# Kernel optimization log

Measured on AMD Instinct MI355X. Metric: run time of the kernel, lower is better.

## Reference

```python
import jax, jax.numpy as jnp
import numpy as np

EPS = 1e-7
MAX_SQDIST = 50.0
K_NEG = 75  # self.nsn / neg_num
GAMMA = 1.0

N_NODES = 30000
DIM = 128
T_LINKS = 3000


def _minkowski_dot(x, y):
    # x, y: (..., d) -> (...,)
    return -x[..., 0] * y[..., 0] + jnp.sum(x[..., 1:] * y[..., 1:], axis=-1)


def _sqdist(x, y, c):
    # Hyperboloid squared distance (HGCN manifolds.Hyperboloid.sqdist)
    K = 1.0 / c
    theta = jnp.clip(-_minkowski_dot(x, y) / K, 1.0 + EPS)
    return jnp.minimum(K * jnp.arccosh(theta) ** 2, MAX_SQDIST)


def _sqdist_all(qx, emb, c):
    # qx: (t, d) queries vs all emb: (N, d) -> (t, N)
    prod = -jnp.outer(qx[:, 0], emb[:, 0]) + qx[:, 1:] @ emb[:, 1:].T
    K = 1.0 / c
    theta = jnp.clip(-prod / K, 1.0 + EPS)
    return jnp.minimum(K * jnp.arccosh(theta) ** 2, MAX_SQDIST)


def setup_inputs() -> dict:
    key = jax.random.key(0)
    k1, k2 = jax.random.split(key)
    embeddings = jax.random.normal(k1, (N_NODES, DIM), dtype=jnp.float32)
    c = jnp.ones((1,), dtype=jnp.float32)
    train_links = jax.random.randint(k2, (T_LINKS, 2), 0, N_NODES, dtype=jnp.int64)
    return {"embeddings": embeddings, "c": c, "train_links": train_links}


def reference(embeddings, c, train_links):
    cs = c[0]
    t = train_links.shape[0]
    k = K_NEG
    left = train_links[:, 0]
    right = train_links[:, 1]
    left_x = embeddings[left]    # (t, d)
    right_x = embeddings[right]  # (t, d)

    # positive sqdist + margin
    D = _sqdist(left_x, right_x, cs) + GAMMA  # (t,)

    # hardest negatives: k nearest nodes to each query (ascending sqdist)
    def knn_idx(qx):
        sq = _sqdist_all(qx, embeddings, cs)       # (t, N)
        _, idx = jax.lax.top_k(-sq, k)             # smallest-k distances
        return idx                                  # (t, k)

    neg_right = knn_idx(left_x)   # negatives replacing right entity
    neg2_left = knn_idx(right_x)  # negatives replacing left entity

    # B = sqdist(left, neg_right); L1 = relu(D - B)
    B = _sqdist(left_x[:, None, :], embeddings[neg_right], cs)   # (t, k)
    L1 = jax.nn.relu(D[:, None] - B)

    # E = sqdist(neg2_left, right); L2 = relu(D - E)
    E = _sqdist(embeddings[neg2_left], right_x[:, None, :], cs)  # (t, k)
    L2 = jax.nn.relu(D[:, None] - E)

    return (jnp.sum(L1) + jnp.sum(L2)) / (2.0 * k * t)
```

## Files before the change

kernel.cpp:

```cpp
#include <hip/hip_runtime.h>
#include <hip/hip_fp16.h>
#include <hip/hip_bf16.h>

#define TL 3000
#define NN 30000
#define DIM 128
#define KNEG 75
#define NQL (2 * TL)
#define EPSF 1e-7f
#define MAXSQ 50.0f

#define ESUB 512
#define ECH 256
#define NCH (ESUB / ECH)
#define QT 64
#define QBLK 94
#define FLAGTH 125

typedef __attribute__((ext_vector_type(8))) short bf16x8;
typedef __attribute__((ext_vector_type(4))) float f32x4;

__device__ __forceinline__ int wred_i(int v) {
#pragma unroll
  for (int o = 32; o > 0; o >>= 1) v += __shfl_xor(v, o, 64);
  return v;
}
__device__ __forceinline__ float wred_f(float v) {
#pragma unroll
  for (int o = 32; o > 0; o >>= 1) v += __shfl_xor(v, o, 64);
  return v;
}

__device__ __forceinline__ float sqdist_f(float prod, float cv, float K) {
  float theta = fmaxf(-prod * cv, 1.0f + EPSF);
  float a = acoshf(theta);
  return fminf(K * a * a, MAXSQ);
}

__device__ __forceinline__ unsigned short to_bf16(float x) {
  __hip_bfloat16 h = __float2bfloat16(x);
  return *(unsigned short*)&h;
}

__launch_bounds__(256)
__global__ void gemm_cf(const float* __restrict__ emb, const float* __restrict__ c,
                        const int* __restrict__ links, float* __restrict__ partial,
                        int* __restrict__ nf, int* __restrict__ list) {
  __shared__ __align__(16) unsigned short Es[ECH * DIM];
  const int tid = threadIdx.x;
  const int lane = tid & 63;
  const int w = tid >> 6;
  const int am = lane & 15;
  const int aq = lane >> 4;
  const int qt = blockIdx.x;
  const float cv = c[0];
  const float K = 1.0f / cv;
  const float thresh = -(1.0f + EPSF) / cv;

  bf16x8 A[4][4];
#pragma unroll
  for (int mg = 0; mg < 4; ++mg) {
    int q = qt * QT + mg * 16 + am;
    int node = 0;
    if (q < NQL) {
      int li = (q < TL) ? q : q - TL;
      node = (q < TL) ? links[2 * li] : links[2 * li + 1];
    }
    const float* qr = emb + (size_t)node * DIM;
#pragma unroll
    for (int kc = 0; kc < 4; ++kc) {
      float4 f0 = *(const float4*)(qr + kc * 32 + aq * 8);
      float4 f1 = *(const float4*)(qr + kc * 32 + aq * 8 + 4);
      if (kc == 0 && aq == 0) f0.x = -f0.x;
      bf16x8 v;
      v[0] = (short)to_bf16(f0.x); v[1] = (short)to_bf16(f0.y);
      v[2] = (short)to_bf16(f0.z); v[3] = (short)to_bf16(f0.w);
      v[4] = (short)to_bf16(f1.x); v[5] = (short)to_bf16(f1.y);
      v[6] = (short)to_bf16(f1.z); v[7] = (short)to_bf16(f1.w);
      A[mg][kc] = v;
    }
  }

  int cnt[4][4];
#pragma unroll
  for (int mg = 0; mg < 4; ++mg)
#pragma unroll
    for (int r = 0; r < 4; ++r) cnt[mg][r] = 0;

  for (int ch = 0; ch < NCH; ++ch) {
#pragma unroll
    for (int i = 0; i < 16; ++i) {
      int g = w * 16 + i;
      int sg = g >> 2, kc = g & 3;
      const float* src = emb + (size_t)(ch * ECH + sg * 16 + am) * DIM + kc * 32 + aq * 8;
      float4 f0 = *(const float4*)src;
      float4 f1 = *(const float4*)(src + 4);
      bf16x8 v;
      v[0] = (short)to_bf16(f0.x); v[1] = (short)to_bf16(f0.y);
      v[2] = (short)to_bf16(f0.z); v[3] = (short)to_bf16(f0.w);
      v[4] = (short)to_bf16(f1.x); v[5] = (short)to_bf16(f1.y);
      v[6] = (short)to_bf16(f1.z); v[7] = (short)to_bf16(f1.w);
      *(bf16x8*)&Es[(g * 64 + lane) * 8] = v;
    }
    __syncthreads();
#pragma unroll
    for (int s = 0; s < 4; ++s) {
      int sg = w * 4 + s;
      f32x4 a0 = {0.f, 0.f, 0.f, 0.f}, a1 = {0.f, 0.f, 0.f, 0.f};
      f32x4 a2 = {0.f, 0.f, 0.f, 0.f}, a3 = {0.f, 0.f, 0.f, 0.f};
#pragma unroll
      for (int kc = 0; kc < 4; ++kc) {
        bf16x8 B = *(const bf16x8*)&Es[((sg * 4 + kc) * 64 + lane) * 8];
        a0 = __builtin_amdgcn_mfma_f32_16x16x32_bf16(A[0][kc], B, a0, 0, 0, 0);
        a1 = __builtin_amdgcn_mfma_f32_16x16x32_bf16(A[1][kc], B, a1, 0, 0, 0);
        a2 = __builtin_amdgcn_mfma_f32_16x16x32_bf16(A[2][kc], B, a2, 0, 0, 0);
        a3 = __builtin_amdgcn_mfma_f32_16x16x32_bf16(A[3][kc], B, a3, 0, 0, 0);
      }
#pragma unroll
      for (int r = 0; r < 4; ++r) {
        cnt[0][r] += (a0[r] >= thresh);
        cnt[1][r] += (a1[r] >= thresh);
        cnt[2][r] += (a2[r] >= thresh);
        cnt[3][r] += (a3[r] >= thresh);
      }
    }
    __syncthreads();
  }

  int* lc = (int*)&Es[0];
  if (tid < QT + 1) lc[tid] = 0;
  __syncthreads();
#pragma unroll
  for (int mg = 0; mg < 4; ++mg)
#pragma unroll
    for (int r = 0; r < 4; ++r) {
      int v = cnt[mg][r];
      v += __shfl_xor(v, 1, 64);
      v += __shfl_xor(v, 2, 64);
      v += __shfl_xor(v, 4, 64);
      v += __shfl_xor(v, 8, 64);
      if (am == 0) atomicAdd(&lc[mg * 16 + aq * 4 + r], v);
    }
  __syncthreads();

  if (tid < QT) {
    float contrib = 0.f;
    int q = qt * QT + tid;
    if (q < NQL) {
      int li = (q < TL) ? q : q - TL;
      long l = links[2 * li];
      long r = links[2 * li + 1];
      const float4* x = (const float4*)(emb + l * DIM);
      const float4* y = (const float4*)(emb + r * DIM);
      float dot = 0.f, x0 = 0.f, y0 = 0.f;
#pragma unroll
      for (int k = 0; k < 32; ++k) {
        float4 a = x[k], b = y[k];
        if (k == 0) { x0 = a.x; y0 = b.x; }
        dot = fmaf(a.x, b.x, dot);
        dot = fmaf(a.y, b.y, dot);
        dot = fmaf(a.z, b.z, dot);
        dot = fmaf(a.w, b.w, dot);
      }
      float Dq = sqdist_f(dot - 2.0f * x0 * y0, cv, K) + 1.0f;
      float acl = acoshf(1.0f + EPSF);
      float clipv = fminf(K * acl * acl, MAXSQ);
      if (lc[tid] >= FLAGTH) {
        contrib = (float)KNEG * fmaxf(Dq - clipv, 0.f);
      } else {
        int p = atomicAdd(&lc[QT], 1);
        list[qt * QT + p] = q;
      }
    }
    contrib = wred_f(contrib);
    if (tid == 0) partial[qt] = contrib * (1.0f / (2.0f * (float)KNEG * (float)TL));
  }
  __syncthreads();
  if (tid == 0) nf[qt] = lc[QT];
}

__launch_bounds__(256)
__global__ void final_kernel(const float* __restrict__ emb, const float* __restrict__ c,
                             const int* __restrict__ links, const float* __restrict__ partial,
                             const int* __restrict__ nf, const int* __restrict__ list,
                             float* __restrict__ out) {
  __shared__ __align__(16) float qvec[DIM];
  __shared__ unsigned short s16[NN];
  __shared__ int ish[4];
  __shared__ float fsh[4];
  __shared__ float acc_total;
  const int tid = threadIdx.x;

  float t = (tid < QBLK) ? partial[tid] : 0.f;
  t = wred_f(t);
  if ((tid & 63) == 0) fsh[tid >> 6] = t;
  __syncthreads();
  if (tid == 0) acc_total = fsh[0] + fsh[1] + fsh[2] + fsh[3];
  __syncthreads();

  const float cv = c[0];
  const float K = 1.0f / cv;

  for (int qt = 0; qt < QBLK; ++qt) {
    int n = nf[qt];
    for (int j = 0; j < n; ++j) {
      const int q = list[qt * QT + j];
      const int li = (q < TL) ? q : q - TL;
      const int node = (q < TL) ? links[2 * li] : links[2 * li + 1];

      float Dq;
      {
        long l = links[2 * li];
        long r = links[2 * li + 1];
        const float4* x = (const float4*)(emb + l * DIM);
        const float4* y = (const float4*)(emb + r * DIM);
        float dot = 0.f, x0 = 0.f, y0 = 0.f;
#pragma unroll
        for (int k = 0; k < 32; ++k) {
          float4 a = x[k], b = y[k];
          if (k == 0) { x0 = a.x; y0 = b.x; }
          dot = fmaf(a.x, b.x, dot);
          dot = fmaf(a.y, b.y, dot);
          dot = fmaf(a.z, b.z, dot);
          dot = fmaf(a.w, b.w, dot);
        }
        Dq = sqdist_f(dot - 2.0f * x0 * y0, cv, K) + 1.0f;
      }

      if (tid < DIM) qvec[tid] = emb[(long)node * DIM + tid];
      __syncthreads();
      const float q0 = qvec[0];
      const float4* q4 = (const float4*)qvec;

      for (int jj = tid; jj < NN; jj += 256) {
        const float4* row = (const float4*)(emb + (long)jj * DIM);
        float acc = 0.f, e0 = 0.f;
#pragma unroll
        for (int k = 0; k < DIM / 4; ++k) {
          float4 e = row[k];
          float4 v = q4[k];
          if (k == 0) e0 = e.x;
          acc = fmaf(e.x, v.x, acc);
          acc = fmaf(e.y, v.y, acc);
          acc = fmaf(e.z, v.z, acc);
          acc = fmaf(e.w, v.w, acc);
        }
        float s = sqdist_f(acc - 2.0f * e0 * q0, cv, K);
        s16[jj] = __half_as_ushort(__float2half_rn(s));
      }
      __syncthreads();

      unsigned int lo = 0, hi = 0xFFFFu;
      while (lo < hi) {
        unsigned int mid = (lo + hi) >> 1;
        int cnt = 0;
        for (int jj = tid; jj < NN; jj += 256) cnt += (s16[jj] <= mid) ? 1 : 0;
        cnt = wred_i(cnt);
        if ((tid & 63) == 0) ish[tid >> 6] = cnt;
        __syncthreads();
        int tot = ish[0] + ish[1] + ish[2] + ish[3];
        if (tot >= KNEG) hi = mid; else lo = mid + 1;
        __syncthreads();
      }
      const unsigned int T = lo;
      const float Tval = __half2float(__ushort_as_half((unsigned short)T));

      int nl = 0;
      float sum = 0.f;
      for (int jj = tid; jj < NN; jj += 256) {
        unsigned short k = s16[jj];
        if ((unsigned int)k < T) {
          nl++;
          sum += fmaxf(Dq - __half2float(__ushort_as_half(k)), 0.f);
        }
      }
      nl = wred_i(nl);
      sum = wred_f(sum);
      if ((tid & 63) == 0) { ish[tid >> 6] = nl; fsh[tid >> 6] = sum; }
      __syncthreads();
      if (tid == 0) {
        int n_less = ish[0] + ish[1] + ish[2] + ish[3];
        float s = fsh[0] + fsh[1] + fsh[2] + fsh[3];
        s += (float)(KNEG - n_less) * fmaxf(Dq - Tval, 0.f);
        acc_total += s * (1.0f / (2.0f * (float)KNEG * (float)TL));
      }
      __syncthreads();
    }
  }
  if (tid == 0) out[0] = acc_total;
}

extern "C" void kernel_launch(void* const* d_in, const int* in_sizes, int n_in,
                              void* d_out, int out_size, void* d_ws, size_t ws_size,
                              hipStream_t stream) {
  const float* emb = (const float*)d_in[0];
  const float* c = (const float*)d_in[1];
  const int* links = (const int*)d_in[2];
  float* out = (float*)d_out;

  float* partial = (float*)d_ws;
  int* nf = (int*)(partial + QBLK);
  int* list = nf + QBLK;

  gemm_cf<<<QBLK, 256, 0, stream>>>(emb, c, links, partial, nf, list);
  final_kernel<<<1, 256, 0, stream>>>(emb, c, links, partial, nf, list, out);
}
```

Measured before the change: 93.24 us.

## Split candidate-count GEMM across four blocks per query tile and merge flags in final kernel

The screening kernel, which counts how many of the first 512 nodes fall at the clipped minimum distance, now splits those nodes into four 128-node slices. Each slice runs in its own block, so the grid grows from 94 to 376 blocks, and the chunk loop and its mid-loop barriers go away. Per-slice counts, the per-query margin D and the clipped contributions are written to workspace. The single-block final kernel then sums the four counts, builds the fallback list and reads D from workspace instead of recomputing it. The intent is to fill more compute units in the screening pass, at the cost of extra workspace traffic and serial flag-merging work in the single-block kernel.

```diff
diff --git a/kernel.cpp b/kernel.cpp
--- a/kernel.cpp
+++ b/kernel.cpp
@@ -11,11 +11,13 @@
 #define MAXSQ 50.0f
 
 #define ESUB 512
-#define ECH 256
-#define NCH (ESUB / ECH)
+#define NSPL 4
+#define ECHS 128
 #define QT 64
 #define QBLK 94
+#define QS (QBLK * QT)
 #define FLAGTH 125
+#define NORM (1.0f / (2.0f * (float)KNEG * (float)TL))
 
 typedef __attribute__((ext_vector_type(8))) short bf16x8;
 typedef __attribute__((ext_vector_type(4))) float f32x4;
@@ -43,16 +45,17 @@
 }
 
 __launch_bounds__(256)
-__global__ void gemm_cf(const float* __restrict__ emb, const float* __restrict__ c,
-                        const int* __restrict__ links, float* __restrict__ partial,
-                        int* __restrict__ nf, int* __restrict__ list) {
-  __shared__ __align__(16) unsigned short Es[ECH * DIM];
+__global__ void count_kernel(const float* __restrict__ emb, const float* __restrict__ c,
+                             const int* __restrict__ links, int* __restrict__ cnt_ws,
+                             float* __restrict__ contrib_ws, float* __restrict__ Dq_ws) {
+  __shared__ __align__(16) unsigned short Es[ECHS * DIM];
   const int tid = threadIdx.x;
   const int lane = tid & 63;
   const int w = tid >> 6;
   const int am = lane & 15;
   const int aq = lane >> 4;
-  const int qt = blockIdx.x;
+  const int qt = blockIdx.x >> 2;
+  const int spl = blockIdx.x & 3;
   const float cv = c[0];
   const float K = 1.0f / cv;
   const float thresh = -(1.0f + EPSF) / cv;
@@ -81,54 +84,52 @@
     }
   }
 
+#pragma unroll
+  for (int i = 0; i < 8; ++i) {
+    int g = w * 8 + i;
+    int sg = g >> 2, kc = g & 3;
+    const float* src = emb + (size_t)(spl * ECHS + sg * 16 + am) * DIM + kc * 32 + aq * 8;
+    float4 f0 = *(const float4*)src;
+    float4 f1 = *(const float4*)(src + 4);
+    bf16x8 v;
+    v[0] = (short)to_bf16(f0.x); v[1] = (short)to_bf16(f0.y);
+    v[2] = (short)to_bf16(f0.z); v[3] = (short)to_bf16(f0.w);
+    v[4] = (short)to_bf16(f1.x); v[5] = (short)to_bf16(f1.y);
+    v[6] = (short)to_bf16(f1.z); v[7] = (short)to_bf16(f1.w);
+    *(bf16x8*)&Es[(g * 64 + lane) * 8] = v;
+  }
+
   int cnt[4][4];
 #pragma unroll
   for (int mg = 0; mg < 4; ++mg)
 #pragma unroll
     for (int r = 0; r < 4; ++r) cnt[mg][r] = 0;
 
-  for (int ch = 0; ch < NCH; ++ch) {
-#pragma unroll
-    for (int i = 0; i < 16; ++i) {
-      int g = w * 16 + i;
-      int sg = g >> 2, kc = g & 3;
-      const float* src = emb + (size_t)(ch * ECH + sg * 16 + am) * DIM + kc * 32 + aq * 8;
-      float4 f0 = *(const float4*)src;
-      float4 f1 = *(const float4*)(src + 4);
-      bf16x8 v;
-      v[0] = (short)to_bf16(f0.x); v[1] = (short)to_bf16(f0.y);
-      v[2] = (short)to_bf16(f0.z); v[3] = (short)to_bf16(f0.w);
-      v[4] = (short)to_bf16(f1.x); v[5] = (short)to_bf16(f1.y);
-      v[6] = (short)to_bf16(f1.z); v[7] = (short)to_bf16(f1.w);
-      *(bf16x8*)&Es[(g * 64 + lane) * 8] = v;
-    }
-    __syncthreads();
-#pragma unroll
-    for (int s = 0; s < 4; ++s) {
-      int sg = w * 4 + s;
-      f32x4 a0 = {0.f, 0.f, 0.f, 0.f}, a1 = {0.f, 0.f, 0.f, 0.f};
-      f32x4 a2 = {0.f, 0.f, 0.f, 0.f}, a3 = {0.f, 0.f, 0.f, 0.f};
-#pragma unroll
-      for (int kc = 0; kc < 4; ++kc) {
-        bf16x8 B = *(const bf16x8*)&Es[((sg * 4 + kc) * 64 + lane) * 8];
-        a0 = __builtin_amdgcn_mfma_f32_16x16x32_bf16(A[0][kc], B, a0, 0, 0, 0);
-        a1 = __builtin_amdgcn_mfma_f32_16x16x32_bf16(A[1][kc], B, a1, 0, 0, 0);
-        a2 = __builtin_amdgcn_mfma_f32_16x16x32_bf16(A[2][kc], B, a2, 0, 0, 0);
-        a3 = __builtin_amdgcn_mfma_f32_16x16x32_bf16(A[3][kc], B, a3, 0, 0, 0);
-      }
-#pragma unroll
-      for (int r = 0; r < 4; ++r) {
-        cnt[0][r] += (a0[r] >= thresh);
-        cnt[1][r] += (a1[r] >= thresh);
-        cnt[2][r] += (a2[r] >= thresh);
-        cnt[3][r] += (a3[r] >= thresh);
-      }
-    }
-    __syncthreads();
-  }
-
+#pragma unroll
+  for (int s2 = 0; s2 < 2; ++s2) {
+    int sg = w * 2 + s2;
+    f32x4 a0 = {0.f, 0.f, 0.f, 0.f}, a1 = {0.f, 0.f, 0.f, 0.f};
+    f32x4 a2 = {0.f, 0.f, 0.f, 0.f}, a3 = {0.f, 0.f, 0.f, 0.f};
+#pragma unroll
+    for (int kc = 0; kc < 4; ++kc) {
+      bf16x8 B = *(const bf16x8*)&Es[((sg * 4 + kc) * 64 + lane) * 8];
+      a0 = __builtin_amdgcn_mfma_f32_16x16x32_bf16(A[0][kc], B, a0, 0, 0, 0);
+      a1 = __builtin_amdgcn_mfma_f32_16x16x32_bf16(A[1][kc], B, a1, 0, 0, 0);
+      a2 = __builtin_amdgcn_mfma_f32_16x16x32_bf16(A[2][kc], B, a2, 0, 0, 0);
+      a3 = __builtin_amdgcn_mfma_f32_16x16x32_bf16(A[3][kc], B, a3, 0, 0, 0);
+    }
+#pragma unroll
+    for (int r = 0; r < 4; ++r) {
+      cnt[0][r] += (a0[r] >= thresh);
+      cnt[1][r] += (a1[r] >= thresh);
+      cnt[2][r] += (a2[r] >= thresh);
+      cnt[3][r] += (a3[r] >= thresh);
+    }
+  }
+
+  __syncthreads();
   int* lc = (int*)&Es[0];
-  if (tid < QT + 1) lc[tid] = 0;
+  if (tid < QT) lc[tid] = 0;
   __syncthreads();
 #pragma unroll
   for (int mg = 0; mg < 4; ++mg)
@@ -142,9 +143,9 @@
       if (am == 0) atomicAdd(&lc[mg * 16 + aq * 4 + r], v);
     }
   __syncthreads();
-
-  if (tid < QT) {
-    float contrib = 0.f;
+  if (tid < QT) cnt_ws[spl * QS + qt * QT + tid] = lc[tid];
+
+  if (spl == 0 && tid < QT) {
     int q = qt * QT + tid;
     if (q < NQL) {
       int li = (q < TL) ? q : q - TL;
@@ -165,129 +166,115 @@
       float Dq = sqdist_f(dot - 2.0f * x0 * y0, cv, K) + 1.0f;
       float acl = acoshf(1.0f + EPSF);
       float clipv = fminf(K * acl * acl, MAXSQ);
-      if (lc[tid] >= FLAGTH) {
-        contrib = (float)KNEG * fmaxf(Dq - clipv, 0.f);
-      } else {
-        int p = atomicAdd(&lc[QT], 1);
-        list[qt * QT + p] = q;
-      }
-    }
-    contrib = wred_f(contrib);
-    if (tid == 0) partial[qt] = contrib * (1.0f / (2.0f * (float)KNEG * (float)TL));
-  }
-  __syncthreads();
-  if (tid == 0) nf[qt] = lc[QT];
+      Dq_ws[q] = Dq;
+      contrib_ws[q] = (float)KNEG * fmaxf(Dq - clipv, 0.f);
+    }
+  }
 }
 
 __launch_bounds__(256)
 __global__ void final_kernel(const float* __restrict__ emb, const float* __restrict__ c,
-                             const int* __restrict__ links, const float* __restrict__ partial,
-                             const int* __restrict__ nf, const int* __restrict__ list,
+                             const int* __restrict__ links, const int* __restrict__ cnt_ws,
+                             const float* __restrict__ contrib_ws,
+                             const float* __restrict__ Dq_ws, int* __restrict__ list_ws,
                              float* __restrict__ out) {
   __shared__ __align__(16) float qvec[DIM];
   __shared__ unsigned short s16[NN];
   __shared__ int ish[4];
   __shared__ float fsh[4];
   __shared__ float acc_total;
+  __shared__ int nflag;
   const int tid = threadIdx.x;
-
-  float t = (tid < QBLK) ? partial[tid] : 0.f;
-  t = wred_f(t);
-  if ((tid & 63) == 0) fsh[tid >> 6] = t;
+  if (tid == 0) nflag = 0;
+  __syncthreads();
+
+  float acc = 0.f;
+  for (int q = tid; q < NQL; q += 256) {
+    int ct = cnt_ws[q] + cnt_ws[QS + q] + cnt_ws[2 * QS + q] + cnt_ws[3 * QS + q];
+    if (ct >= FLAGTH) {
+      acc += contrib_ws[q];
+    } else {
+      int p = atomicAdd(&nflag, 1);
+      list_ws[p] = q;
+    }
+  }
+  acc = wred_f(acc);
+  if ((tid & 63) == 0) fsh[tid >> 6] = acc;
   __syncthreads();
   if (tid == 0) acc_total = fsh[0] + fsh[1] + fsh[2] + fsh[3];
   __syncthreads();
 
   const float cv = c[0];
   const float K = 1.0f / cv;
-
-  for (int qt = 0; qt < QBLK; ++qt) {
-    int n = nf[qt];
-    for (int j = 0; j < n; ++j) {
-      const int q = list[qt * QT + j];
-      const int li = (q < TL) ? q : q - TL;
-      const int node = (q < TL) ? links[2 * li] : links[2 * li + 1];
-
-      float Dq;
-      {
-        long l = links[2 * li];
-        long r = links[2 * li + 1];
-        const float4* x = (const float4*)(emb + l * DIM);
-        const float4* y = (const float4*)(emb + r * DIM);
-        float dot = 0.f, x0 = 0.f, y0 = 0.f;
-#pragma unroll
-        for (int k = 0; k < 32; ++k) {
-          float4 a = x[k], b = y[k];
-          if (k == 0) { x0 = a.x; y0 = b.x; }
-          dot = fmaf(a.x, b.x, dot);
-          dot = fmaf(a.y, b.y, dot);
-          dot = fmaf(a.z, b.z, dot);
-          dot = fmaf(a.w, b.w, dot);
-        }
-        Dq = sqdist_f(dot - 2.0f * x0 * y0, cv, K) + 1.0f;
+  const int nf = nflag;
+
+  for (int it = 0; it < nf; ++it) {
+    const int q = list_ws[it];
+    const int li = (q < TL) ? q : q - TL;
+    const int node = (q < TL) ? links[2 * li] : links[2 * li + 1];
+    const float Dq = Dq_ws[q];
+
+    if (tid < DIM) qvec[tid] = emb[(long)node * DIM + tid];
+    __syncthreads();
+    const float q0 = qvec[0];
+    const float4* q4 = (const float4*)qvec;
+
+    for (int jj = tid; jj < NN; jj += 256) {
+      const float4* row = (const float4*)(emb + (long)jj * DIM);
+      float dacc = 0.f, e0 = 0.f;
+#pragma unroll
+      for (int k = 0; k < DIM / 4; ++k) {
+        float4 e = row[k];
+        float4 v = q4[k];
+        if (k == 0) e0 = e.x;
+        dacc = fmaf(e.x, v.x, dacc);
+        dacc = fmaf(e.y, v.y, dacc);
+        dacc = fmaf(e.z, v.z, dacc);
+        dacc = fmaf(e.w, v.w, dacc);
       }
-
-      if (tid < DIM) qvec[tid] = emb[(long)node * DIM + tid];
+      float s = sqdist_f(dacc - 2.0f * e0 * q0, cv, K);
+      s16[jj] = __half_as_ushort(__float2half_rn(s));
+    }
+    __syncthreads();
+
+    unsigned int lo = 0, hi = 0xFFFFu;
+    while (lo < hi) {
+      unsigned int mid = (lo + hi) >> 1;
+      int cnt = 0;
+      for (int jj = tid; jj < NN; jj += 256) cnt += (s16[jj] <= mid) ? 1 : 0;
+      cnt = wred_i(cnt);
+      if ((tid & 63) == 0) ish[tid >> 6] = cnt;
       __syncthreads();
-      const float q0 = qvec[0];
-      const float4* q4 = (const float4*)qvec;
-
-      for (int jj = tid; jj < NN; jj += 256) {
-        const float4* row = (const float4*)(emb + (long)jj * DIM);
-        float acc = 0.f, e0 = 0.f;
-#pragma unroll
-        for (int k = 0; k < DIM / 4; ++k) {
-          float4 e = row[k];
-          float4 v = q4[k];
-          if (k == 0) e0 = e.x;
-          acc = fmaf(e.x, v.x, acc);
-          acc = fmaf(e.y, v.y, acc);
-          acc = fmaf(e.z, v.z, acc);
-          acc = fmaf(e.w, v.w, acc);
-        }
-        float s = sqdist_f(acc - 2.0f * e0 * q0, cv, K);
-        s16[jj] = __half_as_ushort(__float2half_rn(s));
+      int tot = ish[0] + ish[1] + ish[2] + ish[3];
+      if (tot >= KNEG) hi = mid; else lo = mid + 1;
+      __syncthreads();
+    }
+    const unsigned int T = lo;
+    const float Tval = __half2float(__ushort_as_half((unsigned short)T));
+
+    int nl = 0;
+    float sum = 0.f;
+    for (int jj = tid; jj < NN; jj += 256) {
+      unsigned short k = s16[jj];
+      if ((unsigned int)k < T) {
+        nl++;
+        sum += fmaxf(Dq - __half2float(__ushort_as_half(k)), 0.f);
       }
-      __syncthreads();
-
-      unsigned int lo = 0, hi = 0xFFFFu;
-      while (lo < hi) {
-        unsigned int mid = (lo + hi) >> 1;
-        int cnt = 0;
-        for (int jj = tid; jj < NN; jj += 256) cnt += (s16[jj] <= mid) ? 1 : 0;
-        cnt = wred_i(cnt);
-        if ((tid & 63) == 0) ish[tid >> 6] = cnt;
-        __syncthreads();
-        int tot = ish[0] + ish[1] + ish[2] + ish[3];
-        if (tot >= KNEG) hi = mid; else lo = mid + 1;
-        __syncthreads();
-      }
-      const unsigned int T = lo;
-      const float Tval = __half2float(__ushort_as_half((unsigned short)T));
-
-      int nl = 0;
-      float sum = 0.f;
-      for (int jj = tid; jj < NN; jj += 256) {
-        unsigned short k = s16[jj];
-        if ((unsigned int)k < T) {
-          nl++;
-          sum += fmaxf(Dq - __half2float(__ushort_as_half(k)), 0.f);
-        }
-      }
-      nl = wred_i(nl);
-      sum = wred_f(sum);
-      if ((tid & 63) == 0) { ish[tid >> 6] = nl; fsh[tid >> 6] = sum; }
-      __syncthreads();
-      if (tid == 0) {
-        int n_less = ish[0] + ish[1] + ish[2] + ish[3];
-        float s = fsh[0] + fsh[1] + fsh[2] + fsh[3];
-        s += (float)(KNEG - n_less) * fmaxf(Dq - Tval, 0.f);
-        acc_total += s * (1.0f / (2.0f * (float)KNEG * (float)TL));
-      }
-      __syncthreads();
-    }
-  }
-  if (tid == 0) out[0] = acc_total;
+    }
+    nl = wred_i(nl);
+    sum = wred_f(sum);
+    if ((tid & 63) == 0) { ish[tid >> 6] = nl; fsh[tid >> 6] = sum; }
+    __syncthreads();
+    if (tid == 0) {
+      int n_less = ish[0] + ish[1] + ish[2] + ish[3];
+      float s = fsh[0] + fsh[1] + fsh[2] + fsh[3];
+      s += (float)(KNEG - n_less) * fmaxf(Dq - Tval, 0.f);
+      acc_total += s;
+    }
+    __syncthreads();
+  }
+
+  if (tid == 0) out[0] = acc_total * NORM;
 }
 
 extern "C" void kernel_launch(void* const* d_in, const int* in_sizes, int n_in,
@@ -298,10 +285,12 @@
   const int* links = (const int*)d_in[2];
   float* out = (float*)d_out;
 
-  float* partial = (float*)d_ws;
-  int* nf = (int*)(partial + QBLK);
-  int* list = nf + QBLK;
-
-  gemm_cf<<<QBLK, 256, 0, stream>>>(emb, c, links, partial, nf, list);
-  final_kernel<<<1, 256, 0, stream>>>(emb, c, links, partial, nf, list, out);
-}
+  int* cnt_ws = (int*)d_ws;
+  float* contrib_ws = (float*)(cnt_ws + NSPL * QS);
+  float* Dq_ws = contrib_ws + QS;
+  int* list_ws = (int*)(Dq_ws + QS);
+
+  count_kernel<<<QBLK * NSPL, 256, 0, stream>>>(emb, c, links, cnt_ws, contrib_ws, Dq_ws);
+  final_kernel<<<1, 256, 0, stream>>>(emb, c, links, cnt_ws, contrib_ws, Dq_ws, list_ws,
+                                      out);
+}
```

Measured after the change: 96.77 us. 1.04x slower.
